# Kernel tuning notes

Hardware: AMD Instinct MI355X
Metric: run time of the kernel (lower is better)

## Reference

```python
import jax, jax.numpy as jnp
import numpy as np

INPUT_DIMS = 512
OUTPUT_DIMS = 512
GRID_SIZE = 8


def setup_inputs() -> dict:
    key = jax.random.key(0)
    k_x, k_w = jax.random.split(key)
    x = jax.random.normal(k_x, (4, 2048, INPUT_DIMS), dtype=jnp.float32)
    scale = 1.0 / (np.sqrt(INPUT_DIMS) * np.sqrt(GRID_SIZE))
    fouriercoeffs = jax.random.normal(
        k_w, (2, OUTPUT_DIMS, INPUT_DIMS, GRID_SIZE), dtype=jnp.float32) * scale
    bias = jnp.zeros((1, OUTPUT_DIMS), dtype=jnp.float32)
    return {"x": x, "fouriercoeffs": fouriercoeffs, "bias": bias}


def reference(x, fouriercoeffs, bias):
    out_shape = x.shape[:-1] + (OUTPUT_DIMS,)
    xf = x.reshape(-1, INPUT_DIMS)  # [N, I]
    k = jnp.arange(1, GRID_SIZE + 1, dtype=x.dtype)  # [G]
    arg = xf[:, :, None] * k  # [N, I, G]
    # contract cos/sin features against coeffs: two batched GEMMs
    y = jnp.einsum('nig,oig->no', jnp.cos(arg), fouriercoeffs[0])
    y = y + jnp.einsum('nig,oig->no', jnp.sin(arg), fouriercoeffs[1])
    y = y + bias
    return y.reshape(out_shape)
```

## Files before the change

### kernel.cpp

```cpp
#include <hip/hip_runtime.h>
#include <hip/hip_bf16.h>


typedef __attribute__((ext_vector_type(8))) short s16x8;
typedef __attribute__((ext_vector_type(4))) int   i32x4;
typedef __attribute__((ext_vector_type(4))) float f32x4;

#define NROWS 8192
#define IDIM  512
#define ODIM  512
#define KDIM  8192

static __device__ __forceinline__ short f2bf(float f) {
    union { float f; unsigned u; } v; v.f = f;
    unsigned r = v.u + 0x7fffu + ((v.u >> 16) & 1u);
    return (short)(r >> 16);
}

static __device__ __forceinline__ float bf2f(short h) {
    union { unsigned u; float f; } v;
    v.u = ((unsigned)(unsigned short)h) << 16;
    return v.f;
}

static __device__ __forceinline__ int pkbf(float c, float s) {
    union { __hip_bfloat162 h; int i; } u;
    u.h = __float22bfloat162_rn(make_float2(c, s));
    return u.i;
}

__global__ __launch_bounds__(256) void fkan_prep(const float* __restrict__ cf,
                                                 short* __restrict__ Wb) {
    const int o = blockIdx.x;
    const int tid = threadIdx.x;
#pragma unroll
    for (int rep = 0; rep < 2; ++rep) {
        const int i = tid + rep * 256;
        const float* c0 = cf + (o * 512 + i) * 8;
        const float* c1 = cf + ((512 + o) * 512 + i) * 8;
        float4 a0 = *(const float4*)c0;
        float4 a1 = *(const float4*)(c0 + 4);
        float4 b0 = *(const float4*)c1;
        float4 b1 = *(const float4*)(c1 + 4);
        s16x8 lo, hi;
        lo[0] = f2bf(a0.x); lo[1] = f2bf(b0.x);
        lo[2] = f2bf(a0.y); lo[3] = f2bf(b0.y);
        lo[4] = f2bf(a0.z); lo[5] = f2bf(b0.z);
        lo[6] = f2bf(a0.w); lo[7] = f2bf(b0.w);
        hi[0] = f2bf(a1.x); hi[1] = f2bf(b1.x);
        hi[2] = f2bf(a1.y); hi[3] = f2bf(b1.y);
        hi[4] = f2bf(a1.z); hi[5] = f2bf(b1.z);
        hi[6] = f2bf(a1.w); hi[7] = f2bf(b1.w);
        *(s16x8*)(Wb + o * KDIM + i * 16)     = lo;
        *(s16x8*)(Wb + o * KDIM + i * 16 + 8) = hi;
    }
}

__global__ __launch_bounds__(256, 2) void fkan_gemm9(const float* __restrict__ x,
                                                     const short* __restrict__ Wb,
                                                     short* __restrict__ P) {
    __shared__ short As[2][128 * 40];
    __shared__ short Bs[2][256 * 32];

    const int bid = blockIdx.x;
    const int xcd = bid & 7;
    const int bn = xcd & 1, kc = xcd >> 1;
    const int bm = bid >> 3;
    const int n0 = bm * 128, o0 = bn * 256, i0 = kc * 128;
    const int kbase = i0 * 16;
    const int NKT = 64;

    const int tid = threadIdx.x;
    const int wid = tid >> 6, lane = tid & 63;
    const int lrow = lane & 15, lk = lane >> 4;
    const int wr = wid >> 1, wc = wid & 1;

    f32x4 acc[4][8];
#pragma unroll
    for (int a = 0; a < 4; ++a)
#pragma unroll
        for (int b = 0; b < 8; ++b) {
            f32x4 z = {0.f, 0.f, 0.f, 0.f};
            acc[a][b] = z;
        }

    const int nl = tid >> 1, isel = tid & 1;
    const float* xrow = x + (n0 + nl) * 512 + i0 + isel;

    auto stage = [&](int t, int nb, float xx) {
#pragma unroll
        for (int w = 0; w < 4; ++w) {
            const int ch = w * 256 + tid;
            const int r = ch >> 2, sl = ch & 3;
            const int cb = sl ^ ((r >> 1) & 3);
            const short* src = Wb + (size_t)(o0 + r) * KDIM + kbase + t * 32 + cb * 8;
            short* ldst = &Bs[nb][w * 2048 + wid * 512];
            __builtin_amdgcn_global_load_lds(
                (const __attribute__((address_space(1))) void*)src,
                (__attribute__((address_space(3))) void*)ldst, 16, 0, 0);
        }
        float s1, c1;
        __sincosf(xx, &s1, &c1);
        float c = c1, s = s1;
        i32x4 lo, hi;
#pragma unroll
        for (int g = 0; g < 8; ++g) {
            const int p = pkbf(c, s);
            if (g < 4) lo[g] = p; else hi[g - 4] = p;
            const float t1 = s * s1, t2 = c * s1;
            const float cn = __builtin_fmaf(c, c1, -t1);
            s = __builtin_fmaf(s, c1, t2);
            c = cn;
        }
        short* Ab = As[nb];
        *(i32x4*)&Ab[nl * 40 + (isel * 2) * 8]     = lo;
        *(i32x4*)&Ab[nl * 40 + (isel * 2 + 1) * 8] = hi;
    };

    float xv = xrow[0];
    stage(0, 0, xv);
    xv = xrow[2];
    __syncthreads();

    for (int kt = 0; kt < NKT; ++kt) {
        const int cur = kt & 1;

        s16x8 af[4], bfr[8];
#pragma unroll
        for (int mf = 0; mf < 4; ++mf) {
            const int row = wr * 64 + mf * 16 + lrow;
            af[mf] = *(const s16x8*)&As[cur][row * 40 + lk * 8];
        }
#pragma unroll
        for (int nf = 0; nf < 8; ++nf) {
            const int row = wc * 128 + nf * 16 + lrow;
            const int sl = lk ^ ((row >> 1) & 3);
            bfr[nf] = *(const s16x8*)&Bs[cur][row * 32 + sl * 8];
        }

        if (kt + 1 < NKT) {
            stage(kt + 1, cur ^ 1, xv);
            if (kt + 2 < NKT) xv = xrow[(kt + 2) * 2];
        }

#pragma unroll
        for (int mf = 0; mf < 4; ++mf)
#pragma unroll
            for (int nf = 0; nf < 8; ++nf)
                acc[mf][nf] = __builtin_amdgcn_mfma_f32_16x16x32_bf16(
                    af[mf], bfr[nf], acc[mf][nf], 0, 0, 0);

        __syncthreads();
    }

    unsigned short* dst = (unsigned short*)P + (size_t)kc * (NROWS * ODIM);
#pragma unroll
    for (int nf = 0; nf < 8; ++nf) {
        const int oc = o0 + wc * 128 + nf * 16 + lrow;
#pragma unroll
        for (int mf = 0; mf < 4; ++mf) {
            const f32x4 v = acc[mf][nf];
            const int rbase = n0 + wr * 64 + mf * 16 + lk * 4;
#pragma unroll
            for (int j = 0; j < 4; ++j)
                dst[(size_t)(rbase + j) * 512 + oc] = (unsigned short)f2bf(v[j]);
        }
    }
}

__global__ __launch_bounds__(256) void fkan_combine4(const short* __restrict__ P,
                                                     const float* __restrict__ bias,
                                                     float* __restrict__ out) {
    const int total = NROWS * ODIM;
    const int stride = gridDim.x * 256 * 8;
    for (int e = (blockIdx.x * 256 + threadIdx.x) * 8; e < total; e += stride) {
        s16x8 a = *(const s16x8*)(P + e);
        s16x8 b = *(const s16x8*)(P + total + e);
        s16x8 c = *(const s16x8*)(P + 2 * total + e);
        s16x8 d = *(const s16x8*)(P + 3 * total + e);
        const int col = e & 511;
        float4 c0 = *(const float4*)(bias + col);
        float4 c1 = *(const float4*)(bias + col + 4);
        float4 r0, r1;
        r0.x = (bf2f(a[0]) + bf2f(b[0])) + (bf2f(c[0]) + bf2f(d[0])) + c0.x;
        r0.y = (bf2f(a[1]) + bf2f(b[1])) + (bf2f(c[1]) + bf2f(d[1])) + c0.y;
        r0.z = (bf2f(a[2]) + bf2f(b[2])) + (bf2f(c[2]) + bf2f(d[2])) + c0.z;
        r0.w = (bf2f(a[3]) + bf2f(b[3])) + (bf2f(c[3]) + bf2f(d[3])) + c0.w;
        r1.x = (bf2f(a[4]) + bf2f(b[4])) + (bf2f(c[4]) + bf2f(d[4])) + c1.x;
        r1.y = (bf2f(a[5]) + bf2f(b[5])) + (bf2f(c[5]) + bf2f(d[5])) + c1.y;
        r1.z = (bf2f(a[6]) + bf2f(b[6])) + (bf2f(c[6]) + bf2f(d[6])) + c1.z;
        r1.w = (bf2f(a[7]) + bf2f(b[7])) + (bf2f(c[7]) + bf2f(d[7])) + c1.w;
        *(float4*)(out + e)     = r0;
        *(float4*)(out + e + 4) = r1;
    }
}

__global__ __launch_bounds__(256, 2) void fkan_gemm_fb(const float* __restrict__ x,
                                                       const short* __restrict__ Wb,
                                                       const float* __restrict__ bias,
                                                       float* __restrict__ outp) {
    __shared__ short As[2][128 * 64];
    __shared__ short Bs[2][128 * 64];
    const int bid = blockIdx.x;
    const int xcd = bid & 7, idx = bid >> 3;
    const int bn = xcd & 3, bm = idx + (xcd >> 2) * 32;
    const int n0 = bm * 128, o0 = bn * 128;
    const int tid = threadIdx.x;
    const int wid = tid >> 6, lane = tid & 63;
    const int lrow = lane & 15, lk = lane >> 4;
    const int wr = wid >> 1, wc = wid & 1;
    f32x4 acc[4][4];
#pragma unroll
    for (int a = 0; a < 4; ++a)
#pragma unroll
        for (int b = 0; b < 4; ++b) { f32x4 z = {0,0,0,0}; acc[a][b] = z; }
    const int nl = tid >> 1, isel = tid & 1;
    const float* xrow = x + (n0 + nl) * 512 + isel * 2;
    auto stage = [&](int t, int nb, float2 xvv) {
#pragma unroll
        for (int w = 0; w < 4; ++w) {
            const int chunk = w * 256 + tid;
            const int r = chunk >> 3, pc = chunk & 7;
            const int lc = pc ^ (r & 7);
            const short* src = Wb + (o0 + r) * KDIM + t * 64 + lc * 8;
            short* ldst = &Bs[nb][w * 2048 + wid * 512];
            __builtin_amdgcn_global_load_lds(
                (const __attribute__((address_space(1))) void*)src,
                (__attribute__((address_space(3))) void*)ldst, 16, 0, 0);
        }
#pragma unroll
        for (int ii = 0; ii < 2; ++ii) {
            const float xx = ii ? xvv.y : xvv.x;
            float s1, c1; __sincosf(xx, &s1, &c1);
            float c = c1, s = s1;
            i32x4 lo, hi;
#pragma unroll
            for (int g = 0; g < 8; ++g) {
                const int p = pkbf(c, s);
                if (g < 4) lo[g] = p; else hi[g - 4] = p;
                const float t1 = s * s1, t2 = c * s1;
                const float cn = __builtin_fmaf(c, c1, -t1);
                s = __builtin_fmaf(s, c1, t2); c = cn;
            }
            const int cb0 = (isel * 2 + ii) * 2;
            *(i32x4*)&As[nb][nl * 64 + ((cb0 ^ (nl & 7))) * 8]       = lo;
            *(i32x4*)&As[nb][nl * 64 + (((cb0 + 1) ^ (nl & 7))) * 8] = hi;
        }
    };
    float2 xv = *(const float2*)xrow;
    stage(0, 0, xv);
    xv = *(const float2*)(xrow + 4);
    __syncthreads();
    for (int kt = 0; kt < 128; ++kt) {
        const int cur = kt & 1;
        s16x8 af[2][4], bfr[2][4];
#pragma unroll
        for (int ksub = 0; ksub < 2; ++ksub) {
#pragma unroll
            for (int mf = 0; mf < 4; ++mf) {
                const int row = wr * 64 + mf * 16 + lrow;
                af[ksub][mf] = *(const s16x8*)&As[cur][row * 64 + ((ksub * 4 + lk) ^ (row & 7)) * 8];
            }
#pragma unroll
            for (int nf = 0; nf < 4; ++nf) {
                const int row = wc * 64 + nf * 16 + lrow;
                bfr[ksub][nf] = *(const s16x8*)&Bs[cur][row * 64 + ((ksub * 4 + lk) ^ (row & 7)) * 8];
            }
        }
        if (kt + 1 < 128) {
            stage(kt + 1, cur ^ 1, xv);
            if (kt + 2 < 128) xv = *(const float2*)(xrow + (kt + 2) * 4);
        }
#pragma unroll
        for (int ksub = 0; ksub < 2; ++ksub)
#pragma unroll
            for (int mf = 0; mf < 4; ++mf)
#pragma unroll
                for (int nf = 0; nf < 4; ++nf)
                    acc[mf][nf] = __builtin_amdgcn_mfma_f32_16x16x32_bf16(
                        af[ksub][mf], bfr[ksub][nf], acc[mf][nf], 0, 0, 0);
        __syncthreads();
    }
#pragma unroll
    for (int nf = 0; nf < 4; ++nf) {
        const int oc = o0 + wc * 64 + nf * 16 + lrow;
        const float bv = bias[oc];
#pragma unroll
        for (int mf = 0; mf < 4; ++mf) {
            const f32x4 v = acc[mf][nf];
            const int rbase = n0 + wr * 64 + mf * 16 + lk * 4;
#pragma unroll
            for (int j = 0; j < 4; ++j)
                outp[(size_t)(rbase + j) * 512 + oc] = v[j] + bv;
        }
    }
}

extern "C" void kernel_launch(void* const* d_in, const int* in_sizes, int n_in,
                              void* d_out, int out_size, void* d_ws, size_t ws_size,
                              hipStream_t stream) {
    const float* x    = (const float*)d_in[0];
    const float* cf   = (const float*)d_in[1];
    const float* bias = (const float*)d_in[2];
    float* out = (float*)d_out;

    const size_t partial_bytes = (size_t)4 * NROWS * ODIM * 2;
    const size_t wb_bytes = (size_t)ODIM * KDIM * 2;

    if (ws_size >= partial_bytes + wb_bytes) {
        short* P  = (short*)d_ws;
        short* Wb = (short*)((char*)d_ws + partial_bytes);
        fkan_prep<<<512, 256, 0, stream>>>(cf, Wb);
        fkan_gemm9<<<512, 256, 0, stream>>>(x, Wb, P);
        fkan_combine4<<<2048, 256, 0, stream>>>(P, bias, out);
    } else {
        short* Wb = (short*)d_ws;
        fkan_prep<<<512, 256, 0, stream>>>(cf, Wb);
        fkan_gemm_fb<<<256, 256, 0, stream>>>(x, Wb, bias, out);
    }
}
```

Measured before the change: 93.86 us.

## Switch GEMM to 32x32x16 MFMA with XOR-swizzled paired-row LDS layout

Replaces the 16x16x32 bf16 MFMA tiles with 32x32x16 MFMA tiles, so each wave issues fewer, larger matrix instructions and reloads fragments from LDS less often. The LDS layout of both the A (cos/sin features) and B (weights) tiles changes to pack two rows per 64-element line with an XOR swizzle, which removes the padding on A and is meant to avoid bank conflicts for the new fragment access pattern. The epilogue is rewritten for the 32x32 accumulator register layout. The risk is that the new swizzle or the output indexing is wrong, and that scattered 2-byte partial stores remain in the epilogue.

```diff
diff --git a/kernel.cpp b/kernel.cpp
--- a/kernel.cpp
+++ b/kernel.cpp
@@ -2,9 +2,10 @@
 #include <hip/hip_bf16.h>
 
 
-typedef __attribute__((ext_vector_type(8))) short s16x8;
-typedef __attribute__((ext_vector_type(4))) int   i32x4;
-typedef __attribute__((ext_vector_type(4))) float f32x4;
+typedef __attribute__((ext_vector_type(8)))  short s16x8;
+typedef __attribute__((ext_vector_type(4)))  int   i32x4;
+typedef __attribute__((ext_vector_type(4)))  float f32x4;
+typedef __attribute__((ext_vector_type(16))) float f32x16;
 
 #define NROWS 8192
 #define IDIM  512
@@ -56,11 +57,11 @@
     }
 }
 
-__global__ __launch_bounds__(256, 2) void fkan_gemm9(const float* __restrict__ x,
-                                                     const short* __restrict__ Wb,
-                                                     short* __restrict__ P) {
-    __shared__ short As[2][128 * 40];
-    __shared__ short Bs[2][256 * 32];
+__global__ __launch_bounds__(256, 2) void fkan_gemm10(const float* __restrict__ x,
+                                                      const short* __restrict__ Wb,
+                                                      short* __restrict__ P) {
+    __shared__ short As[2][64 * 64];
+    __shared__ short Bs[2][128 * 64];
 
     const int bid = blockIdx.x;
     const int xcd = bid & 7;
@@ -72,17 +73,16 @@
 
     const int tid = threadIdx.x;
     const int wid = tid >> 6, lane = tid & 63;
-    const int lrow = lane & 15, lk = lane >> 4;
+    const int l32 = lane & 31, hi32 = lane >> 5;
     const int wr = wid >> 1, wc = wid & 1;
 
-    f32x4 acc[4][8];
-#pragma unroll
-    for (int a = 0; a < 4; ++a)
-#pragma unroll
-        for (int b = 0; b < 8; ++b) {
-            f32x4 z = {0.f, 0.f, 0.f, 0.f};
-            acc[a][b] = z;
-        }
+    f32x16 acc[2][4];
+#pragma unroll
+    for (int a = 0; a < 2; ++a)
+#pragma unroll
+        for (int b = 0; b < 4; ++b)
+#pragma unroll
+            for (int e = 0; e < 16; ++e) acc[a][b][e] = 0.f;
 
     const int nl = tid >> 1, isel = tid & 1;
     const float* xrow = x + (n0 + nl) * 512 + i0 + isel;
@@ -91,9 +91,10 @@
 #pragma unroll
         for (int w = 0; w < 4; ++w) {
             const int ch = w * 256 + tid;
-            const int r = ch >> 2, sl = ch & 3;
-            const int cb = sl ^ ((r >> 1) & 3);
-            const short* src = Wb + (size_t)(o0 + r) * KDIM + kbase + t * 32 + cb * 8;
+            const int l = ch >> 3, sl = ch & 7;
+            const int cb = sl ^ (l & 7);
+            const int r = 2 * l + (cb >> 2);
+            const short* src = Wb + (size_t)(o0 + r) * KDIM + kbase + t * 32 + (cb & 3) * 8;
             short* ldst = &Bs[nb][w * 2048 + wid * 512];
             __builtin_amdgcn_global_load_lds(
                 (const __attribute__((address_space(1))) void*)src,
@@ -113,8 +114,10 @@
             c = cn;
         }
         short* Ab = As[nb];
-        *(i32x4*)&Ab[nl * 40 + (isel * 2) * 8]     = lo;
-        *(i32x4*)&Ab[nl * 40 + (isel * 2 + 1) * 8] = hi;
+        const int lA = nl >> 1;
+        const int cb0 = (nl & 1) * 4 + isel * 2;
+        *(i32x4*)&Ab[lA * 64 + ((cb0 ^ (lA & 7))) * 8]       = lo;
+        *(i32x4*)&Ab[lA * 64 + (((cb0 + 1) ^ (lA & 7))) * 8] = hi;
     };
 
     float xv = xrow[0];
@@ -125,18 +128,27 @@
     for (int kt = 0; kt < NKT; ++kt) {
         const int cur = kt & 1;
 
-        s16x8 af[4], bfr[8];
-#pragma unroll
-        for (int mf = 0; mf < 4; ++mf) {
-            const int row = wr * 64 + mf * 16 + lrow;
-            af[mf] = *(const s16x8*)&As[cur][row * 40 + lk * 8];
-        }
-#pragma unroll
-        for (int nf = 0; nf < 8; ++nf) {
-            const int row = wc * 128 + nf * 16 + lrow;
-            const int sl = lk ^ ((row >> 1) & 3);
-            bfr[nf] = *(const s16x8*)&Bs[cur][row * 32 + sl * 8];
-        }
+        s16x8 af[2][2], bfr[4][2];
+#pragma unroll
+        for (int mt = 0; mt < 2; ++mt)
+#pragma unroll
+            for (int ks = 0; ks < 2; ++ks) {
+                const int row = wr * 64 + mt * 32 + l32;
+                const int cch = ks * 2 + hi32;
+                const int l = row >> 1;
+                const int slot = (((row & 1) * 4 + cch) ^ (l & 7));
+                af[mt][ks] = *(const s16x8*)&As[cur][l * 64 + slot * 8];
+            }
+#pragma unroll
+        for (int nt = 0; nt < 4; ++nt)
+#pragma unroll
+            for (int ks = 0; ks < 2; ++ks) {
+                const int row = wc * 128 + nt * 32 + l32;
+                const int cch = ks * 2 + hi32;
+                const int l = row >> 1;
+                const int slot = (((row & 1) * 4 + cch) ^ (l & 7));
+                bfr[nt][ks] = *(const s16x8*)&Bs[cur][l * 64 + slot * 8];
+            }
 
         if (kt + 1 < NKT) {
             stage(kt + 1, cur ^ 1, xv);
@@ -144,28 +156,31 @@
         }
 
 #pragma unroll
-        for (int mf = 0; mf < 4; ++mf)
-#pragma unroll
-            for (int nf = 0; nf < 8; ++nf)
-                acc[mf][nf] = __builtin_amdgcn_mfma_f32_16x16x32_bf16(
-                    af[mf], bfr[nf], acc[mf][nf], 0, 0, 0);
+        for (int ks = 0; ks < 2; ++ks)
+#pragma unroll
+            for (int mt = 0; mt < 2; ++mt)
+#pragma unroll
+                for (int nt = 0; nt < 4; ++nt)
+                    acc[mt][nt] = __builtin_amdgcn_mfma_f32_32x32x16_bf16(
+                        af[mt][ks], bfr[nt][ks], acc[mt][nt], 0, 0, 0);
 
         __syncthreads();
     }
 
     unsigned short* dst = (unsigned short*)P + (size_t)kc * (NROWS * ODIM);
 #pragma unroll
-    for (int nf = 0; nf < 8; ++nf) {
-        const int oc = o0 + wc * 128 + nf * 16 + lrow;
-#pragma unroll
-        for (int mf = 0; mf < 4; ++mf) {
-            const f32x4 v = acc[mf][nf];
-            const int rbase = n0 + wr * 64 + mf * 16 + lk * 4;
-#pragma unroll
-            for (int j = 0; j < 4; ++j)
-                dst[(size_t)(rbase + j) * 512 + oc] = (unsigned short)f2bf(v[j]);
-        }
-    }
+    for (int mt = 0; mt < 2; ++mt)
+#pragma unroll
+        for (int nt = 0; nt < 4; ++nt) {
+            const f32x16 v = acc[mt][nt];
+            const int oc = o0 + wc * 128 + nt * 32 + l32;
+            const int rb = n0 + wr * 64 + mt * 32 + 4 * hi32;
+#pragma unroll
+            for (int reg = 0; reg < 16; ++reg) {
+                const int row = rb + (reg & 3) + 8 * (reg >> 2);
+                dst[(size_t)row * 512 + oc] = (unsigned short)f2bf(v[reg]);
+            }
+        }
 }
 
 __global__ __launch_bounds__(256) void fkan_combine4(const short* __restrict__ P,
@@ -311,7 +326,7 @@
         short* P  = (short*)d_ws;
         short* Wb = (short*)((char*)d_ws + partial_bytes);
         fkan_prep<<<512, 256, 0, stream>>>(cf, Wb);
-        fkan_gemm9<<<512, 256, 0, stream>>>(x, Wb, P);
+        fkan_gemm10<<<512, 256, 0, stream>>>(x, Wb, P);
         fkan_combine4<<<2048, 256, 0, stream>>>(P, bias, out);
     } else {
         short* Wb = (short*)d_ws;
```

Measured after the change: 96.32 us. +2.6%, slower.
